# Performance work log

Measured on AMD Instinct MI355X. Metric: run time of the kernel, lower is better.

## Reference

```python
import jax, jax.numpy as jnp
import numpy as np

B, N, D = 64, 128, 32
P = N * (N - 1)          # ordered pairs
H1, H2, HF = 32, 32, 16  # layer_widths=(32,32), final_widths=(16,)
EPS = 1e-5
SLOPE = 0.01             # LeakyReLU default


def _leaky(x):
    return jnp.where(x >= 0, x, SLOPE * x)


def setup_inputs() -> dict:
    key = jax.random.key(0)
    ks = jax.random.split(key, 16)
    # all ordered pairs (i, j), i != j, grouped by source i
    src = np.repeat(np.arange(N), N - 1)
    tgt = np.array([j for i in range(N) for j in range(N) if j != i])
    s = 0.1
    return {
        "inputs": jax.random.normal(ks[0], (B, N, D), jnp.float32),
        "src": jnp.asarray(src, jnp.int32),
        "tgt": jnp.asarray(tgt, jnp.int32),
        # edge MLP: Linear(2D,32) -> BN1d(P) -> LeakyReLU -> Linear(32,32) -> LeakyReLU -> Linear(32, 1+D)
        "W1": jax.random.normal(ks[1], (2 * D, H1), jnp.float32) * s,
        "b1": jnp.zeros((H1,), jnp.float32),
        "g1": jnp.ones((P,), jnp.float32),
        "be1": jnp.zeros((P,), jnp.float32),
        "W2": jax.random.normal(ks[2], (H1, H2), jnp.float32) * s,
        "b2": jnp.zeros((H2,), jnp.float32),
        "W3": jax.random.normal(ks[3], (H2, 1 + D), jnp.float32) * s,
        "b3": jnp.zeros((1 + D,), jnp.float32),
        # final MLP: Linear(2D,16) -> BN1d(16) -> LeakyReLU -> Linear(16, D)
        "Wf1": jax.random.normal(ks[4], (2 * D, HF), jnp.float32) * s,
        "bf1": jnp.zeros((HF,), jnp.float32),
        "gf": jnp.ones((HF,), jnp.float32),
        "bef": jnp.zeros((HF,), jnp.float32),
        "Wf2": jax.random.normal(ks[5], (HF, D), jnp.float32) * s,
        "bf2": jnp.zeros((D,), jnp.float32),
    }


def reference(inputs, src, tgt, W1, b1, g1, be1, W2, b2, W3, b3,
              Wf1, bf1, gf, bef, Wf2, bf2):
    b, n, d = inputs.shape
    # gather pair features: (B, P, 2D)
    paired = jnp.concatenate([inputs[:, src], inputs[:, tgt]], axis=2)
    h = paired @ W1 + b1                              # (B, P, H1)
    # BatchNorm1d(P) on (B, P, H1): normalize per pair channel over (batch, feat)
    m = h.mean(axis=(0, 2), keepdims=True)
    v = h.var(axis=(0, 2), keepdims=True)
    h = (h - m) * jax.lax.rsqrt(v + EPS) * g1[None, :, None] + be1[None, :, None]
    h = _leaky(h) @ W2 + b2
    h = _leaky(h) @ W3 + b3                           # (B, P, 1+D)
    edges = jax.nn.sigmoid(h[..., :1])                # (B, P, 1)
    messages = h[..., 1:]                             # (B, P, D)
    weighted = edges * messages
    # segment-sum over the (N-1) senders per source node
    agg = weighted.reshape(b, n, n - 1, d).sum(axis=2)  # (B, N, D)
    sm = jnp.concatenate([inputs, agg], axis=2).reshape(-1, 2 * d)
    f = sm @ Wf1 + bf1                                # (B*N, HF)
    mf = f.mean(axis=0)
    vf = f.var(axis=0)
    f = (f - mf) * jax.lax.rsqrt(vf + EPS) * gf + bef
    out = _leaky(f) @ Wf2 + bf2
    return edges[..., 0], out.reshape(b, n, d)
```

## Files before the change

### kernel.cpp

```cpp
#include <hip/hip_runtime.h>
#include <hip/hip_bf16.h>
#include <math.h>

#define BB 64
#define NN 128
#define DD 32
#define PP (NN * (NN - 1))
#define EPSF 1e-5f

typedef __attribute__((ext_vector_type(8))) short bf16x8;
typedef __attribute__((ext_vector_type(4))) float f32x4;

static __device__ __forceinline__ unsigned short f2bf(float x) {
    unsigned u = __builtin_bit_cast(unsigned, x);
    u += 0x7fff + ((u >> 16) & 1);
    return (unsigned short)(u >> 16);
}
static __device__ __forceinline__ float leakyf(float x) {
    return fmaxf(x, 0.01f * x);
}

__global__ __launch_bounds__(256) void proj_kernel(
    const float* __restrict__ inputs, const float* __restrict__ W1,
    const float* __restrict__ b1,
    const float* __restrict__ W2, const float* __restrict__ W3,
    float* __restrict__ AT, float* __restrict__ BT,
    unsigned short* __restrict__ ATh, unsigned short* __restrict__ BTh,
    float* __restrict__ SQp,
    unsigned short* __restrict__ W2p, unsigned short* __restrict__ W3p,
    float* __restrict__ fpartA, float* __restrict__ fpartB)
{
    __shared__ float Xs[16 * 33];
    __shared__ float W1s[2048];
    __shared__ float red[16];

    int tid = threadIdx.x;
    int n = blockIdx.x >> 2, q = blockIdx.x & 3;

    for (int idx = tid; idx < 2048; idx += 256) W1s[idx] = W1[idx];
    for (int idx = tid; idx < 512; idx += 256) {
        int r = idx >> 5, d = idx & 31;
        Xs[r * 33 + d] = inputs[(size_t)(q * 16 + r) * 4096 + n * 32 + d];
    }
    __syncthreads();

    int j = tid & 31, rb = tid >> 5;
    int lane = tid & 63, w = tid >> 6;
    float b1j = b1[j];
    float sa = 0.f, qa = 0.f, sb = 0.f, qb = 0.f;
    #pragma unroll
    for (int i = 0; i < 2; ++i) {
        int r = rb * 2 + i;
        int b = q * 16 + r;
        float a = b1j, c = 0.f;
        #pragma unroll
        for (int k = 0; k < 32; ++k) {
            float x = Xs[r * 33 + k];
            a += x * W1s[k * 32 + j];
            c += x * W1s[(32 + k) * 32 + j];
        }
        size_t off = ((size_t)n * 64 + b) * 32 + j;
        AT[off] = a;  BT[off] = c;
        ATh[off] = f2bf(a);  BTh[off] = f2bf(c);
        sa += a; qa += a * a; sb += c; qb += c * c;
    }
    #pragma unroll
    for (int d = 32; d > 0; d >>= 1) {
        sa += __shfl_down(sa, d, 64);
        qa += __shfl_down(qa, d, 64);
        sb += __shfl_down(sb, d, 64);
        qb += __shfl_down(qb, d, 64);
    }
    if (lane == 0) { red[w*4+0] = sa; red[w*4+1] = qa; red[w*4+2] = sb; red[w*4+3] = qb; }
    __syncthreads();
    if (tid == 0) {
        float4 v;
        v.x = red[0] + red[4] + red[8]  + red[12];
        v.y = red[1] + red[5] + red[9]  + red[13];
        v.z = red[2] + red[6] + red[10] + red[14];
        v.w = red[3] + red[7] + red[11] + red[15];
        ((float4*)SQp)[n * 4 + q] = v;
    }

    if (blockIdx.x == 0 && tid < 64) {
        int l = tid, nn2 = l & 15, kc = l >> 4;
        #pragma unroll
        for (int ct = 0; ct < 2; ++ct)
            #pragma unroll
            for (int jj = 0; jj < 8; ++jj) {
                int k = kc * 8 + jj;
                W2p[(ct * 64 + l) * 8 + jj] = f2bf(W2[k * 32 + ct * 16 + nn2]);
            }
        #pragma unroll
        for (int ct = 0; ct < 3; ++ct)
            #pragma unroll
            for (int jj = 0; jj < 8; ++jj) {
                int k = kc * 8 + jj;
                int c2 = ct * 16 + nn2;
                W3p[(ct * 64 + l) * 8 + jj] = f2bf(c2 < 33 ? W3[k * 33 + c2] : 0.f);
            }
    }
    if (blockIdx.x == 1) {
        for (int idx = tid; idx < 1024; idx += 256) {
            fpartA[idx] = 0.f;
            fpartB[idx] = 0.f;
        }
    }
}

__global__ __launch_bounds__(256) void stats2_kernel(
    const unsigned short* __restrict__ ATh, const unsigned short* __restrict__ BTh,
    const float* __restrict__ SQp,
    const float* __restrict__ g1, const float* __restrict__ be1,
    float* __restrict__ statA, float* __restrict__ statB)
{
    __shared__ __align__(16) float part[4 * 64 * 4];
    int tid = threadIdx.x;
    int lane = tid & 63, w = tid >> 6;
    int s0 = (blockIdx.x >> 3) * 16, t0 = (blockIdx.x & 7) * 16;

    int m = lane & 15, kc = lane >> 4;
    const unsigned short* abase = ATh + (size_t)(s0 + m) * 2048 + kc * 8 + w * 512;
    const unsigned short* bbase = BTh + (size_t)(t0 + m) * 2048 + kc * 8 + w * 512;

    f32x4 acc0 = {0.f, 0.f, 0.f, 0.f}, acc1 = {0.f, 0.f, 0.f, 0.f};
    #pragma unroll
    for (int step = 0; step < 8; ++step) {
        bf16x8 av0 = *(const bf16x8*)(abase + (2 * step) * 32);
        bf16x8 bv0 = *(const bf16x8*)(bbase + (2 * step) * 32);
        acc0 = __builtin_amdgcn_mfma_f32_16x16x32_bf16(av0, bv0, acc0, 0, 0, 0);
        bf16x8 av1 = *(const bf16x8*)(abase + (2 * step + 1) * 32);
        bf16x8 bv1 = *(const bf16x8*)(bbase + (2 * step + 1) * 32);
        acc1 = __builtin_amdgcn_mfma_f32_16x16x32_bf16(av1, bv1, acc1, 0, 0, 0);
    }
    f32x4 acc;
    acc[0] = acc0[0] + acc1[0]; acc[1] = acc0[1] + acc1[1];
    acc[2] = acc0[2] + acc1[2]; acc[3] = acc0[3] + acc1[3];
    *(f32x4*)&part[(w * 64 + lane) * 4] = acc;
    __syncthreads();

    if (w == 0) {
        #pragma unroll
        for (int ww = 1; ww < 4; ++ww) {
            f32x4 o2 = *(const f32x4*)&part[(ww * 64 + lane) * 4];
            acc[0] += o2[0]; acc[1] += o2[1]; acc[2] += o2[2]; acc[3] += o2[3];
        }
        int col = lane & 15, quad = lane >> 4;
        int t = t0 + col;
        float sbt = 0.f, qbt = 0.f;
        #pragma unroll
        for (int o2 = 0; o2 < 4; ++o2) {
            float4 v = ((const float4*)SQp)[t * 4 + o2];
            sbt += v.z; qbt += v.w;
        }
        #pragma unroll
        for (int r = 0; r < 4; ++r) {
            int s = s0 + quad * 4 + r;
            if (s != t) {
                float sas = 0.f, qas = 0.f;
                #pragma unroll
                for (int o2 = 0; o2 < 4; ++o2) {
                    float4 v = ((const float4*)SQp)[s * 4 + o2];
                    sas += v.x; qas += v.y;
                }
                int e = t - (t > s);
                int p = s * 127 + e;
                float S = sas + sbt;
                float Q = qas + qbt + 2.f * acc[r];
                float mean = S * (1.f / 2048.f);
                float var  = Q * (1.f / 2048.f) - mean * mean;
                float inv  = rsqrtf(var + EPSF);
                float sc   = inv * g1[p];
                statA[p] = sc;
                statB[p] = be1[p] - mean * sc;
            }
        }
    }
}

__global__ __launch_bounds__(256) void edges_kernel(
    const float* __restrict__ AT, const float* __restrict__ BT,
    const float* __restrict__ statA, const float* __restrict__ statB,
    const unsigned short* __restrict__ W2p, const unsigned short* __restrict__ W3p,
    const float* __restrict__ b2, const float* __restrict__ b3,
    const float* __restrict__ inputs, const float* __restrict__ Wf1,
    const float* __restrict__ bf1,
    float* __restrict__ edges_out,
    float* __restrict__ f, float* __restrict__ fpartA, float* __restrict__ fpartB)
{
    __shared__ __align__(16) unsigned short Abuf[4096];
    __shared__ __align__(16) unsigned short Hbuf[4096];
    __shared__ float Wf1s[1024];
    __shared__ float aggbuf[4][32];

    int tid = threadIdx.x;
    int s = blockIdx.x & 127;
    int o = blockIdx.x >> 7;
    int lane = tid & 63, w = tid >> 6;

    for (int idx = tid; idx < 1024; idx += 256) Wf1s[idx] = Wf1[idx];

    int e2 = tid >> 1;
    int half = tid & 1;
    int k0 = half * 16;
    int m = e2 & 15, r = e2 >> 4;
    int L0 = 2 * half * 16 + m;
    bool valid = (e2 < 127);
    int t = valid ? (e2 + (e2 >= s)) : 0;
    int pe = s * 127 + (valid ? e2 : 126);
    float sc = 0.f, sh = 0.f;
    if (valid) { sc = statA[pe]; sh = statB[pe]; }

    int col = lane & 15, q4 = (lane >> 4) * 4;
    int qbase = lane & 48;
    bf16x8 wb2[2], wb3[3];
    wb2[0] = *(const bf16x8*)(W2p + (0 * 64 + lane) * 8);
    wb2[1] = *(const bf16x8*)(W2p + (1 * 64 + lane) * 8);
    wb3[0] = *(const bf16x8*)(W3p + (0 * 64 + lane) * 8);
    wb3[1] = *(const bf16x8*)(W3p + (1 * 64 + lane) * 8);
    wb3[2] = *(const bf16x8*)(W3p + (2 * 64 + lane) * 8);
    float b2c0 = b2[col], b2c1 = b2[16 + col];
    float b3c[3];
    #pragma unroll
    for (int ct = 0; ct < 3; ++ct) {
        int c = ct * 16 + col;
        b3c[ct] = (c < 33) ? b3[c] : 0.f;
    }

    for (int bi = 0; bi < 4; ++bi) {
        int b = o * 4 + bi;
        __syncthreads();

        float nh[16];
        if (valid) {
            const float4* brow = (const float4*)(BT + ((size_t)t * 64 + b) * 32 + k0);
            const float4* ar4  = (const float4*)(AT + ((size_t)s * 64 + b) * 32 + k0);
            #pragma unroll
            for (int q = 0; q < 4; ++q) {
                float4 bv = brow[q];
                float4 av = ar4[q];
                nh[4*q+0] = leakyf((av.x + bv.x) * sc + sh);
                nh[4*q+1] = leakyf((av.y + bv.y) * sc + sh);
                nh[4*q+2] = leakyf((av.z + bv.z) * sc + sh);
                nh[4*q+3] = leakyf((av.w + bv.w) * sc + sh);
            }
        } else {
            #pragma unroll
            for (int q = 0; q < 16; ++q) nh[q] = 0.f;
        }
        bf16x8 v0, v1;
        #pragma unroll
        for (int jj = 0; jj < 8; ++jj) {
            v0[jj] = (short)f2bf(nh[jj]);
            v1[jj] = (short)f2bf(nh[8 + jj]);
        }
        *(bf16x8*)&Abuf[((size_t)r * 64 + L0) * 8]      = v0;
        *(bf16x8*)&Abuf[((size_t)r * 64 + L0 + 16) * 8] = v1;
        __syncthreads();

        #pragma unroll
        for (int rt = 0; rt < 2; ++rt) {
            int r2 = w * 2 + rt;
            bf16x8 a = *(const bf16x8*)&Abuf[((size_t)r2 * 64 + lane) * 8];
            f32x4 c0 = {0.f, 0.f, 0.f, 0.f}, c1 = {0.f, 0.f, 0.f, 0.f};
            c0 = __builtin_amdgcn_mfma_f32_16x16x32_bf16(a, wb2[0], c0, 0, 0, 0);
            c1 = __builtin_amdgcn_mfma_f32_16x16x32_bf16(a, wb2[1], c1, 0, 0, 0);
            #pragma unroll
            for (int reg = 0; reg < 4; ++reg) {
                float x = leakyf(c0[reg] + b2c0);
                int c = col;
                Hbuf[((size_t)r2 * 64 + (c >> 3) * 16 + q4 + reg) * 8 + (c & 7)] = f2bf(x);
                float y = leakyf(c1[reg] + b2c1);
                int c2 = 16 + col;
                Hbuf[((size_t)r2 * 64 + (c2 >> 3) * 16 + q4 + reg) * 8 + (c2 & 7)] = f2bf(y);
            }
        }
        __syncthreads();

        f32x4 oo[2][3];
        #pragma unroll
        for (int rt = 0; rt < 2; ++rt) {
            int r2 = w * 2 + rt;
            bf16x8 a2 = *(const bf16x8*)&Hbuf[((size_t)r2 * 64 + lane) * 8];
            #pragma unroll
            for (int ct = 0; ct < 3; ++ct) {
                f32x4 cc = {0.f, 0.f, 0.f, 0.f};
                oo[rt][ct] = __builtin_amdgcn_mfma_f32_16x16x32_bf16(a2, wb3[ct], cc, 0, 0, 0);
            }
        }

        float ev[2][4];
        #pragma unroll
        for (int rt = 0; rt < 2; ++rt) {
            int row0 = (w * 2 + rt) * 16 + q4;
            float e0 = 0.f, e1 = 0.f, e2v = 0.f, e3 = 0.f;
            if (col == 0) {
                e0  = 1.f / (1.f + __expf(-(oo[rt][0][0] + b3c[0])));
                e1  = 1.f / (1.f + __expf(-(oo[rt][0][1] + b3c[0])));
                e2v = 1.f / (1.f + __expf(-(oo[rt][0][2] + b3c[0])));
                e3  = 1.f / (1.f + __expf(-(oo[rt][0][3] + b3c[0])));
                float* ep = edges_out + (size_t)b * PP + s * 127 + row0;
                ep[0] = e0; ep[1] = e1; ep[2] = e2v;
                if (row0 != 124) ep[3] = e3;
            }
            ev[rt][0] = __shfl(e0,  qbase, 64);
            ev[rt][1] = __shfl(e1,  qbase, 64);
            ev[rt][2] = __shfl(e2v, qbase, 64);
            ev[rt][3] = __shfl(e3,  qbase, 64);
            if (row0 == 124) ev[rt][3] = 0.f;
        }

        #pragma unroll
        for (int ct = 0; ct < 3; ++ct) {
            int c = ct * 16 + col;
            if (c >= 1 && c <= 32) {
                float part = 0.f;
                #pragma unroll
                for (int rt = 0; rt < 2; ++rt) {
                    float bb3 = b3c[ct];
                    part += ev[rt][0] * (oo[rt][ct][0] + bb3);
                    part += ev[rt][1] * (oo[rt][ct][1] + bb3);
                    part += ev[rt][2] * (oo[rt][ct][2] + bb3);
                    part += ev[rt][3] * (oo[rt][ct][3] + bb3);
                }
                part += __shfl_xor(part, 16, 64);
                part += __shfl_xor(part, 32, 64);
                if ((lane >> 4) == 0) aggbuf[w][c - 1] = part;
            }
        }
        __syncthreads();

        size_t row = (size_t)b * 128 + s;
        if (tid < 32) {
            float tot = aggbuf[0][tid] + aggbuf[1][tid] + aggbuf[2][tid] + aggbuf[3][tid];
            aggbuf[0][tid] = tot;
        }
        if (tid < 16) {
            const float* xrow = inputs + row * 32;
            float acc = bf1[tid];
            #pragma unroll
            for (int k = 0; k < 32; ++k) acc += xrow[k] * Wf1s[k * 16 + tid];
            #pragma unroll
            for (int k = 0; k < 32; ++k) acc += aggbuf[0][k] * Wf1s[(32 + k) * 16 + tid];
            f[row * 16 + tid] = acc;
            int bucket = ((blockIdx.x << 2) + bi) & 63;
            atomicAdd(&fpartA[bucket * 16 + tid], acc);
            atomicAdd(&fpartB[bucket * 16 + tid], acc * acc);
        }
    }
}

__global__ __launch_bounds__(256) void out_kernel(
    const float* __restrict__ f,
    const float* __restrict__ fpartA, const float* __restrict__ fpartB,
    const float* __restrict__ gf, const float* __restrict__ bef,
    const float* __restrict__ Wf2, const float* __restrict__ bf2,
    float* __restrict__ outp)
{
    __shared__ float Wf2s[512];
    __shared__ float sc[16], sh[16];
    __shared__ float fs[128];

    int tid = threadIdx.x;
    for (int idx = tid; idx < 512; idx += 256) Wf2s[idx] = Wf2[idx];
    if (tid < 16) {
        float S = 0.f, Q = 0.f;
        #pragma unroll
        for (int g = 0; g < 64; ++g) {
            S += fpartA[g * 16 + tid];
            Q += fpartB[g * 16 + tid];
        }
        float mean = S * (1.f / 8192.f);
        float var  = Q * (1.f / 8192.f) - mean * mean;
        float inv  = rsqrtf(var + EPSF);
        float s2   = inv * gf[tid];
        sc[tid] = s2;
        sh[tid] = bef[tid] - mean * s2;
    }
    int row0 = blockIdx.x * 8;
    if (tid < 128) {
        int r = tid >> 4, j = tid & 15;
        fs[r * 16 + j] = f[(size_t)(row0 + r) * 16 + j];
    }
    __syncthreads();

    int rl = tid >> 5, d = tid & 31;
    float acc = bf2[d];
    #pragma unroll
    for (int j = 0; j < 16; ++j) {
        float v = fs[rl * 16 + j] * sc[j] + sh[j];
        v = leakyf(v);
        acc += v * Wf2s[j * 32 + d];
    }
    outp[(size_t)(row0 + rl) * 32 + d] = acc;
}

extern "C" void kernel_launch(void* const* d_in, const int* in_sizes, int n_in,
                              void* d_out, int out_size, void* d_ws, size_t ws_size,
                              hipStream_t stream) {
    const float* inputs = (const float*)d_in[0];
    const float* W1   = (const float*)d_in[3];
    const float* b1   = (const float*)d_in[4];
    const float* g1   = (const float*)d_in[5];
    const float* be1  = (const float*)d_in[6];
    const float* W2   = (const float*)d_in[7];
    const float* b2   = (const float*)d_in[8];
    const float* W3   = (const float*)d_in[9];
    const float* b3   = (const float*)d_in[10];
    const float* Wf1  = (const float*)d_in[11];
    const float* bf1  = (const float*)d_in[12];
    const float* gf   = (const float*)d_in[13];
    const float* bef  = (const float*)d_in[14];
    const float* Wf2  = (const float*)d_in[15];
    const float* bf2  = (const float*)d_in[16];

    float* ws = (float*)d_ws;
    float* AT     = ws;
    float* BT     = ws + 262144;
    unsigned short* ATh = (unsigned short*)(ws + 524288);
    unsigned short* BTh = ATh + 262144;
    float* SQp    = ws + 786432;
    float* statA  = ws + 790528;
    float* statB  = ws + 806784;
    float* f      = ws + 823040;
    float* fpartA = ws + 954112;
    float* fpartB = ws + 955136;
    unsigned short* W2p = (unsigned short*)(ws + 956160);
    unsigned short* W3p = W2p + 1024;

    float* edges_out = (float*)d_out;
    float* outp      = edges_out + (size_t)BB * PP;

    proj_kernel<<<512, 256, 0, stream>>>(inputs, W1, b1, W2, W3,
                                         AT, BT, ATh, BTh, SQp,
                                         W2p, W3p, fpartA, fpartB);
    stats2_kernel<<<64, 256, 0, stream>>>(ATh, BTh, SQp, g1, be1, statA, statB);
    edges_kernel<<<2048, 256, 0, stream>>>(AT, BT, statA, statB, W2p, W3p,
                                           b2, b3, inputs, Wf1, bf1,
                                           edges_out, f, fpartA, fpartB);
    out_kernel<<<1024, 256, 0, stream>>>(f, fpartA, fpartB, gf, bef, Wf2, bf2, outp);
}
```

Before: 145.3 us.

## Process two batches per edges block with fewer barriers and double grid

Each edges_kernel block now handles two batch entries instead of four, so the grid doubles to 4096 blocks. The two batches are staged together in doubled LDS buffers, which removes per-batch __syncthreads and lets their MFMA work interleave. Float-to-bf16 packing switches to a paired intrinsic, and the final projection runs 32 threads at once instead of 16. The cost is more LDS per block and re-loading the weights and Wf1 in twice as many blocks.

```diff
diff --git a/kernel.cpp b/kernel.cpp
--- a/kernel.cpp
+++ b/kernel.cpp
@@ -15,6 +15,13 @@
     unsigned u = __builtin_bit_cast(unsigned, x);
     u += 0x7fff + ((u >> 16) & 1);
     return (unsigned short)(u >> 16);
+}
+static __device__ __forceinline__ unsigned pk2bf(float a, float b) {
+    float2 t; t.x = a; t.y = b;
+    __hip_bfloat162 h = __float22bfloat162_rn(t);
+    unsigned u;
+    __builtin_memcpy(&u, &h, 4);
+    return u;
 }
 static __device__ __forceinline__ float leakyf(float x) {
     return fmaxf(x, 0.01f * x);
@@ -188,14 +195,14 @@
     float* __restrict__ edges_out,
     float* __restrict__ f, float* __restrict__ fpartA, float* __restrict__ fpartB)
 {
-    __shared__ __align__(16) unsigned short Abuf[4096];
-    __shared__ __align__(16) unsigned short Hbuf[4096];
+    __shared__ __align__(16) unsigned short Abuf[2 * 8 * 64 * 8];
+    __shared__ __align__(16) unsigned short Hbuf[2 * 8 * 64 * 8];
     __shared__ float Wf1s[1024];
-    __shared__ float aggbuf[4][32];
+    __shared__ float aggbuf[2][4][32];
 
     int tid = threadIdx.x;
     int s = blockIdx.x & 127;
-    int o = blockIdx.x >> 7;
+    int b0 = (blockIdx.x >> 7) * 2;
     int lane = tid & 63, w = tid >> 6;
 
     for (int idx = tid; idx < 1024; idx += 256) Wf1s[idx] = Wf1[idx];
@@ -227,10 +234,9 @@
         b3c[ct] = (c < 33) ? b3[c] : 0.f;
     }
 
-    for (int bi = 0; bi < 4; ++bi) {
-        int b = o * 4 + bi;
-        __syncthreads();
-
+    #pragma unroll
+    for (int bsel = 0; bsel < 2; ++bsel) {
+        int b = b0 + bsel;
         float nh[16];
         if (valid) {
             const float4* brow = (const float4*)(BT + ((size_t)t * 64 + b) * 32 + k0);
@@ -248,40 +254,52 @@
             #pragma unroll
             for (int q = 0; q < 16; ++q) nh[q] = 0.f;
         }
-        bf16x8 v0, v1;
-        #pragma unroll
-        for (int jj = 0; jj < 8; ++jj) {
-            v0[jj] = (short)f2bf(nh[jj]);
-            v1[jj] = (short)f2bf(nh[8 + jj]);
-        }
-        *(bf16x8*)&Abuf[((size_t)r * 64 + L0) * 8]      = v0;
-        *(bf16x8*)&Abuf[((size_t)r * 64 + L0 + 16) * 8] = v1;
-        __syncthreads();
-
+        union { bf16x8 v; unsigned u[4]; } U0, U1;
+        #pragma unroll
+        for (int q = 0; q < 4; ++q) {
+            U0.u[q] = pk2bf(nh[2*q],     nh[2*q+1]);
+            U1.u[q] = pk2bf(nh[8+2*q],   nh[8+2*q+1]);
+        }
+        *(bf16x8*)&Abuf[((size_t)(bsel * 8 + r) * 64 + L0) * 8]      = U0.v;
+        *(bf16x8*)&Abuf[((size_t)(bsel * 8 + r) * 64 + L0 + 16) * 8] = U1.v;
+    }
+    __syncthreads();
+
+    #pragma unroll
+    for (int bsel = 0; bsel < 2; ++bsel) {
         #pragma unroll
         for (int rt = 0; rt < 2; ++rt) {
             int r2 = w * 2 + rt;
-            bf16x8 a = *(const bf16x8*)&Abuf[((size_t)r2 * 64 + lane) * 8];
+            bf16x8 a = *(const bf16x8*)&Abuf[((size_t)(bsel * 8 + r2) * 64 + lane) * 8];
             f32x4 c0 = {0.f, 0.f, 0.f, 0.f}, c1 = {0.f, 0.f, 0.f, 0.f};
             c0 = __builtin_amdgcn_mfma_f32_16x16x32_bf16(a, wb2[0], c0, 0, 0, 0);
             c1 = __builtin_amdgcn_mfma_f32_16x16x32_bf16(a, wb2[1], c1, 0, 0, 0);
             #pragma unroll
-            for (int reg = 0; reg < 4; ++reg) {
-                float x = leakyf(c0[reg] + b2c0);
+            for (int reg = 0; reg < 2; ++reg) {
+                float x0 = leakyf(c0[2*reg]   + b2c0);
+                float x1 = leakyf(c0[2*reg+1] + b2c0);
+                float y0 = leakyf(c1[2*reg]   + b2c1);
+                float y1 = leakyf(c1[2*reg+1] + b2c1);
                 int c = col;
-                Hbuf[((size_t)r2 * 64 + (c >> 3) * 16 + q4 + reg) * 8 + (c & 7)] = f2bf(x);
-                float y = leakyf(c1[reg] + b2c1);
+                int base = (bsel * 8 + r2) * 64;
+                Hbuf[((size_t)base + (c >> 3) * 16 + q4 + 2*reg)     * 8 + (c & 7)] = f2bf(x0);
+                Hbuf[((size_t)base + (c >> 3) * 16 + q4 + 2*reg + 1) * 8 + (c & 7)] = f2bf(x1);
                 int c2 = 16 + col;
-                Hbuf[((size_t)r2 * 64 + (c2 >> 3) * 16 + q4 + reg) * 8 + (c2 & 7)] = f2bf(y);
-            }
-        }
-        __syncthreads();
-
+                Hbuf[((size_t)base + (c2 >> 3) * 16 + q4 + 2*reg)     * 8 + (c2 & 7)] = f2bf(y0);
+                Hbuf[((size_t)base + (c2 >> 3) * 16 + q4 + 2*reg + 1) * 8 + (c2 & 7)] = f2bf(y1);
+            }
+        }
+    }
+    __syncthreads();
+
+    #pragma unroll
+    for (int bsel = 0; bsel < 2; ++bsel) {
+        int b = b0 + bsel;
         f32x4 oo[2][3];
         #pragma unroll
         for (int rt = 0; rt < 2; ++rt) {
             int r2 = w * 2 + rt;
-            bf16x8 a2 = *(const bf16x8*)&Hbuf[((size_t)r2 * 64 + lane) * 8];
+            bf16x8 a2 = *(const bf16x8*)&Hbuf[((size_t)(bsel * 8 + r2) * 64 + lane) * 8];
             #pragma unroll
             for (int ct = 0; ct < 3; ++ct) {
                 f32x4 cc = {0.f, 0.f, 0.f, 0.f};
@@ -325,28 +343,29 @@
                 }
                 part += __shfl_xor(part, 16, 64);
                 part += __shfl_xor(part, 32, 64);
-                if ((lane >> 4) == 0) aggbuf[w][c - 1] = part;
-            }
-        }
-        __syncthreads();
-
-        size_t row = (size_t)b * 128 + s;
-        if (tid < 32) {
-            float tot = aggbuf[0][tid] + aggbuf[1][tid] + aggbuf[2][tid] + aggbuf[3][tid];
-            aggbuf[0][tid] = tot;
-        }
-        if (tid < 16) {
-            const float* xrow = inputs + row * 32;
-            float acc = bf1[tid];
-            #pragma unroll
-            for (int k = 0; k < 32; ++k) acc += xrow[k] * Wf1s[k * 16 + tid];
-            #pragma unroll
-            for (int k = 0; k < 32; ++k) acc += aggbuf[0][k] * Wf1s[(32 + k) * 16 + tid];
-            f[row * 16 + tid] = acc;
-            int bucket = ((blockIdx.x << 2) + bi) & 63;
-            atomicAdd(&fpartA[bucket * 16 + tid], acc);
-            atomicAdd(&fpartB[bucket * 16 + tid], acc * acc);
-        }
+                if ((lane >> 4) == 0) aggbuf[bsel][w][c - 1] = part;
+            }
+        }
+    }
+    __syncthreads();
+
+    if (tid < 32) {
+        int bsel = tid >> 4, j = tid & 15;
+        size_t row = (size_t)(b0 + bsel) * 128 + s;
+        const float* xrow = inputs + row * 32;
+        float acc = bf1[j];
+        #pragma unroll
+        for (int k = 0; k < 32; ++k) acc += xrow[k] * Wf1s[k * 16 + j];
+        #pragma unroll
+        for (int k = 0; k < 32; ++k) {
+            float tot = aggbuf[bsel][0][k] + aggbuf[bsel][1][k]
+                      + aggbuf[bsel][2][k] + aggbuf[bsel][3][k];
+            acc += tot * Wf1s[(32 + k) * 16 + j];
+        }
+        f[row * 16 + j] = acc;
+        int bucket = ((blockIdx.x << 1) + bsel) & 63;
+        atomicAdd(&fpartA[bucket * 16 + j], acc);
+        atomicAdd(&fpartB[bucket * 16 + j], acc * acc);
     }
 }
 
@@ -435,7 +454,7 @@
                                          AT, BT, ATh, BTh, SQp,
                                          W2p, W3p, fpartA, fpartB);
     stats2_kernel<<<64, 256, 0, stream>>>(ATh, BTh, SQp, g1, be1, statA, statB);
-    edges_kernel<<<2048, 256, 0, stream>>>(AT, BT, statA, statB, W2p, W3p,
+    edges_kernel<<<4096, 256, 0, stream>>>(AT, BT, statA, statB, W2p, W3p,
                                            b2, b3, inputs, Wf1, bf1,
                                            edges_out, f, fpartA, fpartB);
     out_kernel<<<1024, 256, 0, stream>>>(f, fpartA, fpartB, gf, bef, Wf2, bf2, outp);
```

Result: no change. 145.0 us (-0.2%).

## Restructure edges kernel to one batch per block with register-built MFMA fragments

Applied to the files above, without the earlier changes.

The edges kernel now launches one block per (batch, source) pair instead of looping over four batches per block. Each lane loads its own first-layer activations directly into MFMA A-fragment layout, so the shared Abuf staging and its barriers go away. The hidden layer goes through a small per-wave swizzled LDS tile with no block-wide syncs. Segment-sum partials are accumulated in registers across row tiles, and bf16 packing uses the paired conversion intrinsic. This trades fewer barriers and more parallelism for four times as many blocks, more Wf1 reloads per block, and more atomics on the f statistics buckets.

```diff
diff --git a/kernel.cpp b/kernel.cpp
--- a/kernel.cpp
+++ b/kernel.cpp
@@ -15,6 +15,13 @@
     unsigned u = __builtin_bit_cast(unsigned, x);
     u += 0x7fff + ((u >> 16) & 1);
     return (unsigned short)(u >> 16);
+}
+static __device__ __forceinline__ unsigned pk2bf(float a, float b) {
+    float2 t; t.x = a; t.y = b;
+    __hip_bfloat162 h = __float22bfloat162_rn(t);
+    unsigned u;
+    __builtin_memcpy(&u, &h, 4);
+    return u;
 }
 static __device__ __forceinline__ float leakyf(float x) {
     return fmaxf(x, 0.01f * x);
@@ -188,31 +195,22 @@
     float* __restrict__ edges_out,
     float* __restrict__ f, float* __restrict__ fpartA, float* __restrict__ fpartB)
 {
-    __shared__ __align__(16) unsigned short Abuf[4096];
-    __shared__ __align__(16) unsigned short Hbuf[4096];
+    __shared__ __align__(16) unsigned short Hs[4][512];
     __shared__ float Wf1s[1024];
     __shared__ float aggbuf[4][32];
 
     int tid = threadIdx.x;
     int s = blockIdx.x & 127;
-    int o = blockIdx.x >> 7;
+    int b = blockIdx.x >> 7;
     int lane = tid & 63, w = tid >> 6;
+    int m = lane & 15;
+    int kb = lane >> 4;
+    int col = m;
+    int q4 = kb * 4;
+    int qbase = lane & 48;
 
     for (int idx = tid; idx < 1024; idx += 256) Wf1s[idx] = Wf1[idx];
 
-    int e2 = tid >> 1;
-    int half = tid & 1;
-    int k0 = half * 16;
-    int m = e2 & 15, r = e2 >> 4;
-    int L0 = 2 * half * 16 + m;
-    bool valid = (e2 < 127);
-    int t = valid ? (e2 + (e2 >= s)) : 0;
-    int pe = s * 127 + (valid ? e2 : 126);
-    float sc = 0.f, sh = 0.f;
-    if (valid) { sc = statA[pe]; sh = statB[pe]; }
-
-    int col = lane & 15, q4 = (lane >> 4) * 4;
-    int qbase = lane & 48;
     bf16x8 wb2[2], wb3[3];
     wb2[0] = *(const bf16x8*)(W2p + (0 * 64 + lane) * 8);
     wb2[1] = *(const bf16x8*)(W2p + (1 * 64 + lane) * 8);
@@ -227,126 +225,115 @@
         b3c[ct] = (c < 33) ? b3[c] : 0.f;
     }
 
-    for (int bi = 0; bi < 4; ++bi) {
-        int b = o * 4 + bi;
-        __syncthreads();
-
-        float nh[16];
-        if (valid) {
-            const float4* brow = (const float4*)(BT + ((size_t)t * 64 + b) * 32 + k0);
-            const float4* ar4  = (const float4*)(AT + ((size_t)s * 64 + b) * 32 + k0);
+    const float4* asl = (const float4*)(AT + ((size_t)s * 64 + b) * 32 + kb * 8);
+    float4 a0 = asl[0], a1 = asl[1];
+
+    float aggpart[3] = {0.f, 0.f, 0.f};
+
+    #pragma unroll
+    for (int rt = 0; rt < 2; ++rt) {
+        int tile = w * 2 + rt;
+        int e = tile * 16 + m;
+        bool valid = (e < 127);
+        int ee = valid ? e : 0;
+        int t = ee + (ee >= s);
+        int p = s * 127 + ee;
+        float sc = statA[p], sh = statB[p];
+
+        const float4* bsl = (const float4*)(BT + ((size_t)t * 64 + b) * 32 + kb * 8);
+        float4 bv0 = bsl[0], bv1 = bsl[1];
+
+        float nh[8];
+        nh[0] = leakyf((a0.x + bv0.x) * sc + sh);
+        nh[1] = leakyf((a0.y + bv0.y) * sc + sh);
+        nh[2] = leakyf((a0.z + bv0.z) * sc + sh);
+        nh[3] = leakyf((a0.w + bv0.w) * sc + sh);
+        nh[4] = leakyf((a1.x + bv1.x) * sc + sh);
+        nh[5] = leakyf((a1.y + bv1.y) * sc + sh);
+        nh[6] = leakyf((a1.z + bv1.z) * sc + sh);
+        nh[7] = leakyf((a1.w + bv1.w) * sc + sh);
+        if (!valid) {
             #pragma unroll
-            for (int q = 0; q < 4; ++q) {
-                float4 bv = brow[q];
-                float4 av = ar4[q];
-                nh[4*q+0] = leakyf((av.x + bv.x) * sc + sh);
-                nh[4*q+1] = leakyf((av.y + bv.y) * sc + sh);
-                nh[4*q+2] = leakyf((av.z + bv.z) * sc + sh);
-                nh[4*q+3] = leakyf((av.w + bv.w) * sc + sh);
-            }
-        } else {
-            #pragma unroll
-            for (int q = 0; q < 16; ++q) nh[q] = 0.f;
-        }
-        bf16x8 v0, v1;
-        #pragma unroll
-        for (int jj = 0; jj < 8; ++jj) {
-            v0[jj] = (short)f2bf(nh[jj]);
-            v1[jj] = (short)f2bf(nh[8 + jj]);
-        }
-        *(bf16x8*)&Abuf[((size_t)r * 64 + L0) * 8]      = v0;
-        *(bf16x8*)&Abuf[((size_t)r * 64 + L0 + 16) * 8] = v1;
-        __syncthreads();
-
-        #pragma unroll
-        for (int rt = 0; rt < 2; ++rt) {
-            int r2 = w * 2 + rt;
-            bf16x8 a = *(const bf16x8*)&Abuf[((size_t)r2 * 64 + lane) * 8];
-            f32x4 c0 = {0.f, 0.f, 0.f, 0.f}, c1 = {0.f, 0.f, 0.f, 0.f};
-            c0 = __builtin_amdgcn_mfma_f32_16x16x32_bf16(a, wb2[0], c0, 0, 0, 0);
-            c1 = __builtin_amdgcn_mfma_f32_16x16x32_bf16(a, wb2[1], c1, 0, 0, 0);
-            #pragma unroll
-            for (int reg = 0; reg < 4; ++reg) {
-                float x = leakyf(c0[reg] + b2c0);
-                int c = col;
-                Hbuf[((size_t)r2 * 64 + (c >> 3) * 16 + q4 + reg) * 8 + (c & 7)] = f2bf(x);
-                float y = leakyf(c1[reg] + b2c1);
-                int c2 = 16 + col;
-                Hbuf[((size_t)r2 * 64 + (c2 >> 3) * 16 + q4 + reg) * 8 + (c2 & 7)] = f2bf(y);
-            }
-        }
-        __syncthreads();
-
-        f32x4 oo[2][3];
-        #pragma unroll
-        for (int rt = 0; rt < 2; ++rt) {
-            int r2 = w * 2 + rt;
-            bf16x8 a2 = *(const bf16x8*)&Hbuf[((size_t)r2 * 64 + lane) * 8];
-            #pragma unroll
-            for (int ct = 0; ct < 3; ++ct) {
-                f32x4 cc = {0.f, 0.f, 0.f, 0.f};
-                oo[rt][ct] = __builtin_amdgcn_mfma_f32_16x16x32_bf16(a2, wb3[ct], cc, 0, 0, 0);
-            }
-        }
-
-        float ev[2][4];
-        #pragma unroll
-        for (int rt = 0; rt < 2; ++rt) {
-            int row0 = (w * 2 + rt) * 16 + q4;
-            float e0 = 0.f, e1 = 0.f, e2v = 0.f, e3 = 0.f;
-            if (col == 0) {
-                e0  = 1.f / (1.f + __expf(-(oo[rt][0][0] + b3c[0])));
-                e1  = 1.f / (1.f + __expf(-(oo[rt][0][1] + b3c[0])));
-                e2v = 1.f / (1.f + __expf(-(oo[rt][0][2] + b3c[0])));
-                e3  = 1.f / (1.f + __expf(-(oo[rt][0][3] + b3c[0])));
-                float* ep = edges_out + (size_t)b * PP + s * 127 + row0;
-                ep[0] = e0; ep[1] = e1; ep[2] = e2v;
-                if (row0 != 124) ep[3] = e3;
-            }
-            ev[rt][0] = __shfl(e0,  qbase, 64);
-            ev[rt][1] = __shfl(e1,  qbase, 64);
-            ev[rt][2] = __shfl(e2v, qbase, 64);
-            ev[rt][3] = __shfl(e3,  qbase, 64);
-            if (row0 == 124) ev[rt][3] = 0.f;
-        }
-
+            for (int q = 0; q < 8; ++q) nh[q] = 0.f;
+        }
+        union { bf16x8 v; unsigned u[4]; } AF;
+        #pragma unroll
+        for (int q = 0; q < 4; ++q) AF.u[q] = pk2bf(nh[2*q], nh[2*q+1]);
+
+        f32x4 c0 = {0.f, 0.f, 0.f, 0.f}, c1 = {0.f, 0.f, 0.f, 0.f};
+        c0 = __builtin_amdgcn_mfma_f32_16x16x32_bf16(AF.v, wb2[0], c0, 0, 0, 0);
+        c1 = __builtin_amdgcn_mfma_f32_16x16x32_bf16(AF.v, wb2[1], c1, 0, 0, 0);
+
+        #pragma unroll
+        for (int reg = 0; reg < 4; ++reg) {
+            int row = q4 + reg;
+            float x = leakyf(c0[reg] + b2c0);
+            float y = leakyf(c1[reg] + b2c1);
+            int cA = col;
+            int cB = col + 16;
+            Hs[w][row * 32 + (((cA >> 3) ^ (row >> 2)) & 3) * 8 + (cA & 7)] = f2bf(x);
+            Hs[w][row * 32 + (((cB >> 3) ^ (row >> 2)) & 3) * 8 + (cB & 7)] = f2bf(y);
+        }
+        bf16x8 a2 = *(const bf16x8*)&Hs[w][m * 32 + ((kb ^ (m >> 2)) & 3) * 8];
+
+        f32x4 oo[3];
         #pragma unroll
         for (int ct = 0; ct < 3; ++ct) {
-            int c = ct * 16 + col;
-            if (c >= 1 && c <= 32) {
-                float part = 0.f;
-                #pragma unroll
-                for (int rt = 0; rt < 2; ++rt) {
-                    float bb3 = b3c[ct];
-                    part += ev[rt][0] * (oo[rt][ct][0] + bb3);
-                    part += ev[rt][1] * (oo[rt][ct][1] + bb3);
-                    part += ev[rt][2] * (oo[rt][ct][2] + bb3);
-                    part += ev[rt][3] * (oo[rt][ct][3] + bb3);
-                }
-                part += __shfl_xor(part, 16, 64);
-                part += __shfl_xor(part, 32, 64);
-                if ((lane >> 4) == 0) aggbuf[w][c - 1] = part;
-            }
-        }
-        __syncthreads();
-
+            f32x4 cc = {0.f, 0.f, 0.f, 0.f};
+            oo[ct] = __builtin_amdgcn_mfma_f32_16x16x32_bf16(a2, wb3[ct], cc, 0, 0, 0);
+        }
+
+        float v0 = 0.f, v1 = 0.f, v2 = 0.f, v3 = 0.f;
+        int grow0 = tile * 16 + q4;
+        if (col == 0) {
+            v0 = 1.f / (1.f + __expf(-(oo[0][0] + b3c[0])));
+            v1 = 1.f / (1.f + __expf(-(oo[0][1] + b3c[0])));
+            v2 = 1.f / (1.f + __expf(-(oo[0][2] + b3c[0])));
+            v3 = (grow0 == 124) ? 0.f
+               : 1.f / (1.f + __expf(-(oo[0][3] + b3c[0])));
+            float* ep = edges_out + (size_t)b * PP + s * 127 + grow0;
+            ep[0] = v0; ep[1] = v1; ep[2] = v2;
+            if (grow0 != 124) ep[3] = v3;
+        }
+        float ev0 = __shfl(v0, qbase, 64);
+        float ev1 = __shfl(v1, qbase, 64);
+        float ev2 = __shfl(v2, qbase, 64);
+        float ev3 = __shfl(v3, qbase, 64);
+
+        #pragma unroll
+        for (int ct = 0; ct < 3; ++ct) {
+            float bb3 = b3c[ct];
+            float pt = ev0 * (oo[ct][0] + bb3) + ev1 * (oo[ct][1] + bb3)
+                     + ev2 * (oo[ct][2] + bb3) + ev3 * (oo[ct][3] + bb3);
+            aggpart[ct] += pt;
+        }
+    }
+
+    #pragma unroll
+    for (int ct = 0; ct < 3; ++ct) {
+        float pt = aggpart[ct];
+        pt += __shfl_xor(pt, 16, 64);
+        pt += __shfl_xor(pt, 32, 64);
+        int c = ct * 16 + col;
+        if (kb == 0 && c >= 1 && c <= 32) aggbuf[w][c - 1] = pt;
+    }
+    __syncthreads();
+
+    if (tid < 16) {
         size_t row = (size_t)b * 128 + s;
-        if (tid < 32) {
-            float tot = aggbuf[0][tid] + aggbuf[1][tid] + aggbuf[2][tid] + aggbuf[3][tid];
-            aggbuf[0][tid] = tot;
-        }
-        if (tid < 16) {
-            const float* xrow = inputs + row * 32;
-            float acc = bf1[tid];
-            #pragma unroll
-            for (int k = 0; k < 32; ++k) acc += xrow[k] * Wf1s[k * 16 + tid];
-            #pragma unroll
-            for (int k = 0; k < 32; ++k) acc += aggbuf[0][k] * Wf1s[(32 + k) * 16 + tid];
-            f[row * 16 + tid] = acc;
-            int bucket = ((blockIdx.x << 2) + bi) & 63;
-            atomicAdd(&fpartA[bucket * 16 + tid], acc);
-            atomicAdd(&fpartB[bucket * 16 + tid], acc * acc);
-        }
+        const float* xrow = inputs + row * 32;
+        float acc = bf1[tid];
+        #pragma unroll
+        for (int k = 0; k < 32; ++k) acc += xrow[k] * Wf1s[k * 16 + tid];
+        #pragma unroll
+        for (int k = 0; k < 32; ++k) {
+            float tot = aggbuf[0][k] + aggbuf[1][k] + aggbuf[2][k] + aggbuf[3][k];
+            acc += tot * Wf1s[(32 + k) * 16 + tid];
+        }
+        f[row * 16 + tid] = acc;
+        int bucket = blockIdx.x & 63;
+        atomicAdd(&fpartA[bucket * 16 + tid], acc);
+        atomicAdd(&fpartB[bucket * 16 + tid], acc * acc);
     }
 }
 
@@ -435,7 +422,7 @@
                                          AT, BT, ATh, BTh, SQp,
                                          W2p, W3p, fpartA, fpartB);
     stats2_kernel<<<64, 256, 0, stream>>>(ATh, BTh, SQp, g1, be1, statA, statB);
-    edges_kernel<<<2048, 256, 0, stream>>>(AT, BT, statA, statB, W2p, W3p,
+    edges_kernel<<<8192, 256, 0, stream>>>(AT, BT, statA, statB, W2p, W3p,
                                            b2, b3, inputs, Wf1, bf1,
                                            edges_out, f, fpartA, fpartB);
     out_kernel<<<1024, 256, 0, stream>>>(f, fpartA, fpartB, gf, bef, Wf2, bf2, outp);
```

After: 142.7 us. Within noise of the previous version (-1.8%).
